# Kernel tuning notes

Hardware: AMD Instinct MI355X
Metric: run time of the kernel (lower is better)

## Reference

```python
import jax, jax.numpy as jnp
import numpy as np

W = 5      # window size
H = 4      # num heads (num_channels)
EPS = 1e-6

def rmsnorm(x, w):
    return x * w * jax.lax.rsqrt(jnp.mean(x * x, axis=-1, keepdims=True) + EPS)

def dwconv3d(x, k):
    # x: [B,D0,D1,D2,C], k: [3,3,3,1,C] depthwise 3x3x3 conv, SAME padding
    return jax.lax.conv_general_dilated(
        x, k, (1, 1, 1), 'SAME',
        dimension_numbers=('NDHWC', 'DHWIO', 'NDHWC'),
        feature_group_count=x.shape[-1])

def _part(t):
    # [B,D0,D1,D2,C] -> [B*nw, W^3, C] non-overlapping 3D windows
    B, D0, D1, D2, C = t.shape
    t = t.reshape(B, D0 // W, W, D1 // W, W, D2 // W, W, C)
    t = t.transpose(0, 1, 3, 5, 2, 4, 6, 7)
    return t.reshape(-1, W ** 3, C)

def _unpart(t, B, D0, D1, D2):
    C = t.shape[-1]
    t = t.reshape(B, D0 // W, D1 // W, D2 // W, W, W, W, C)
    t = t.transpose(0, 1, 4, 2, 5, 3, 6, 7)
    return t.reshape(B, D0, D1, D2, C)

def _pool01(t):
    # mean-pool poolable_dims=(0,1) by factor W -> coarse grid
    B, D0, D1, D2, C = t.shape
    return t.reshape(B, D0 // W, W, D1 // W, W, D2, C).mean(axis=(2, 4))

def _mha(q, k, v):
    # q,k,v: [N, L, C] -> [N, L, C] multi-head attention
    N, L, C = q.shape
    dh = C // H
    q = q.reshape(N, L, H, dh)
    k = k.reshape(N, L, H, dh)
    v = v.reshape(N, L, H, dh)
    s = jnp.einsum('nqhd,nkhd->nhqk', q, k) * (1.0 / np.sqrt(dh))
    p = jax.nn.softmax(s, axis=-1)
    return jnp.einsum('nhqk,nkhd->nqhd', p, v).reshape(N, L, C)

def _hier_attn(x, qkv_w, qkv_b, proj_w, proj_b, dw_pre, dw_post, lr_down, lr_up):
    B, D0, D1, D2, C = x.shape
    # conv_position='both': pre depthwise-conv positional term
    xin = x + dwconv3d(x, dw_pre)
    qkv = xin @ qkv_w + qkv_b                     # [B,D0,D1,D2,3C]
    q, k, v = jnp.split(qkv, 3, axis=-1)
    # fine scale: windowed local attention in W^3 blocks
    fine = _unpart(_mha(_part(q), _part(k), _part(v)), B, D0, D1, D2)
    # coarse scale: pool dims (0,1) by W, global attention over coarse tokens
    qc, kc, vc = _pool01(q), _pool01(k), _pool01(v)
    Nc = qc.shape[1] * qc.shape[2] * qc.shape[3]
    oc = _mha(qc.reshape(B, Nc, C), kc.reshape(B, Nc, C), vc.reshape(B, Nc, C))
    oc = oc.reshape(B, D0 // W, D1 // W, D2, C)
    oc = jnp.repeat(jnp.repeat(oc, W, axis=1), W, axis=2)   # upsample to full grid
    # lowrank hierarchical merge of coarse branch into fine branch
    merged = fine + (oc @ lr_down) @ lr_up
    out = merged @ proj_w + proj_b
    out = out + xin                               # attn_residual
    out = out + dwconv3d(out, dw_post)            # post conv position
    return out

def setup_inputs() -> dict:
    key = jax.random.key(0)
    ks = jax.random.split(key, 8)
    B, D0, D1, D2, C = 4, 40, 40, 20, 256
    rank = C // 4
    s = 0.02
    return {
        'x': jax.random.normal(ks[0], (B, D0, D1, D2, C), jnp.float32),
        'norm1_w': jnp.ones((C,), jnp.float32),
        'attn_norm_w': jnp.ones((C,), jnp.float32),
        'qkv_w': jax.random.normal(ks[1], (C, 3 * C), jnp.float32) * s,
        'qkv_b': jnp.zeros((3 * C,), jnp.float32),
        'proj_w': jax.random.normal(ks[2], (C, C), jnp.float32) * s,
        'proj_b': jnp.zeros((C,), jnp.float32),
        'dw_pre': jax.random.normal(ks[3], (3, 3, 3, 1, C), jnp.float32) * s,
        'dw_post': jax.random.normal(ks[4], (3, 3, 3, 1, C), jnp.float32) * s,
        'lr_down': jax.random.normal(ks[5], (C, rank), jnp.float32) * s,
        'lr_up': jax.random.normal(ks[6], (rank, C), jnp.float32) * s,
    }

def reference(x, norm1_w, attn_norm_w, qkv_w, qkv_b, proj_w, proj_b,
              dw_pre, dw_post, lr_down, lr_up) -> jnp.ndarray:
    # x = x + attn_norm(hier_attn(norm1(x)))   (dropout inactive in eval)
    a = _hier_attn(rmsnorm(x, norm1_w), qkv_w, qkv_b, proj_w, proj_b,
                   dw_pre, dw_post, lr_down, lr_up)
    return x + rmsnorm(a, attn_norm_w)
```

## Files before the change

kernel.cpp:

```cpp
#include <hip/hip_runtime.h>

#define D0c 40
#define D1c 40
#define D2c 20
#define NVOX 128000

typedef __attribute__((ext_vector_type(4))) float f4;
typedef __attribute__((ext_vector_type(8))) __bf16 bf8;
typedef __attribute__((ext_vector_type(8))) unsigned short u8s;

static __device__ __forceinline__ unsigned short f2bf(float f) {
  union { float f; unsigned int u; } v; v.f = f;
  unsigned int r = v.u + 0x7fffu + ((v.u >> 16) & 1u);
  return (unsigned short)(r >> 16);
}
static __device__ __forceinline__ float bf2f(unsigned short h) {
  union { unsigned int u; float f; } v; v.u = ((unsigned int)h) << 16;
  return v.f;
}

#define MFMA16(a, b, c) __builtin_amdgcn_mfma_f32_16x16x32_bf16((a), (b), (c), 0, 0, 0)

static __device__ __forceinline__ void gload16(const void* g, void* l) {
  __builtin_amdgcn_global_load_lds((const __attribute__((address_space(1))) unsigned int*)g,
                                   (__attribute__((address_space(3))) unsigned int*)l, 16, 0, 0);
}

#define CONV_LOAD(NB, R)                                                      \
  do {                                                                        \
    _Pragma("unroll") for (int c = 0; c < 9; c++)                             \
        NB[c] = *(const ushort4*)(base[c] + (size_t)(R) * 256);               \
  } while (0)

#define CONV_CONSUME(NB)                                                      \
  do {                                                                        \
    f4 cf[9];                                                                 \
    _Pragma("unroll") for (int c = 0; c < 9; c++) {                           \
      cf[c].x = bf2f(NB[c].x); cf[c].y = bf2f(NB[c].y);                       \
      cf[c].z = bf2f(NB[c].z); cf[c].w = bf2f(NB[c].w);                       \
    }                                                                         \
    _Pragma("unroll") for (int c = 0; c < 9; c++) {                           \
      const f4 w0 = *(const f4*)&wl[(c * 3 + 0) * 256 + c0];                  \
      const f4 w1 = *(const f4*)&wl[(c * 3 + 1) * 256 + c0];                  \
      const f4 w2 = *(const f4*)&wl[(c * 3 + 2) * 256 + c0];                  \
      a0 += w2 * cf[c]; a1 += w1 * cf[c]; a2 += w0 * cf[c];                   \
    }                                                                         \
    a1 += cf[4];                                                              \
  } while (0)

#define CONV_SHIFT()                                                          \
  do { a0 = a1; a1 = a2; a2 = (f4){0.f, 0.f, 0.f, 0.f}; } while (0)

__global__ __launch_bounds__(256) void k_prepw(const float* __restrict__ qkv_w,
                                               const float* __restrict__ proj_w,
                                               unsigned short* __restrict__ wq,
                                               unsigned short* __restrict__ wp,
                                               unsigned short* __restrict__ zpad) {
  if (blockIdx.x == 1024) {
    u8s z = {0, 0, 0, 0, 0, 0, 0, 0};
    for (int i = threadIdx.x; i < 768; i += 256) *(u8s*)(zpad + i * 8) = z;
    return;
  }
  int id = blockIdx.x * 256 + threadIdx.x;
  if (id < 768 * 256) {
    int kk = id & 31, row = (id >> 5) & 127, kc = (id >> 12) & 7, nt = id >> 15;
    int s = kk >> 3, kj = kk & 7;
    int g = s ^ ((row >> 1) & 3);
    int k = kc * 32 + g * 8 + kj;
    int n = nt * 128 + row;
    wq[id] = f2bf(qkv_w[k * 768 + n]);
  } else {
    int j = id - 768 * 256;
    int kk = j & 31, row = (j >> 5) & 127, kc = (j >> 12) & 7, nt = j >> 15;
    int s = kk >> 3, kj = kk & 7;
    int g = s ^ ((row >> 1) & 3);
    int k = kc * 32 + g * 8 + kj;
    int n = nt * 128 + row;
    wp[j] = f2bf(proj_w[k * 256 + n]);
  }
}

__global__ __launch_bounds__(256) void k_rms1(const float* __restrict__ x,
                                              const float* __restrict__ w,
                                              unsigned short* __restrict__ xn) {
  int wv = threadIdx.x >> 6, ln = threadIdx.x & 63;
  int n = blockIdx.x * 4 + wv;
  f4 v = ((const f4*)(x + (size_t)n * 256))[ln];
  float ss = v.x * v.x + v.y * v.y + v.z * v.z + v.w * v.w;
#pragma unroll
  for (int m = 32; m >= 1; m >>= 1) ss += __shfl_xor(ss, m);
  float rs = rsqrtf(ss * (1.f / 256.f) + 1e-6f);
  f4 wv4 = ((const f4*)w)[ln];
  ushort4 o;
  o.x = f2bf(v.x * wv4.x * rs); o.y = f2bf(v.y * wv4.y * rs);
  o.z = f2bf(v.z * wv4.z * rs); o.w = f2bf(v.w * wv4.w * rs);
  ((ushort4*)(xn + (size_t)n * 256))[ln] = o;
}

__global__ __launch_bounds__(256) void k_convpre(const unsigned short* __restrict__ xn,
                                                 const float* __restrict__ dw,
                                                 const unsigned short* __restrict__ zpad,
                                                 unsigned short* __restrict__ xin) {
  __shared__ float wl[6912];
  for (int i = threadIdx.x; i < 6912; i += 256) wl[i] = dw[i];
  __syncthreads();
  int wv = threadIdx.x >> 6, ln = threadIdx.x & 63;
  int col = blockIdx.x * 4 + wv;
  int z1 = col % D1c; int t = col / D1c; int z0 = t % D0c; int b = t / D0c;
  int c0 = ln * 4;

  const unsigned short* base[9];
#pragma unroll
  for (int c = 0; c < 9; c++) {
    int dy = c / 3 - 1, dx = c % 3 - 1;
    int y0 = z0 + dy, y1 = z1 + dx;
    bool valid = ((unsigned)y0 < (unsigned)D0c) && ((unsigned)y1 < (unsigned)D1c);
    base[c] = valid ? (xn + ((size_t)((b * D0c + y0) * D1c + y1) * D2c) * 256 + c0)
                    : (zpad + c0);
  }
  f4 a0 = {0.f,0.f,0.f,0.f}, a1 = {0.f,0.f,0.f,0.f}, a2 = {0.f,0.f,0.f,0.f};
  ushort4 n0[9], n1[9];
  CONV_LOAD(n0, 0);
  CONV_LOAD(n1, 1);
  unsigned short* op = xin + ((size_t)col * D2c) * 256 + c0;

  CONV_CONSUME(n0);
  CONV_SHIFT();
  CONV_LOAD(n0, 2);
  CONV_CONSUME(n1);
  {
    ushort4 o;
    o.x = f2bf(a0.x); o.y = f2bf(a0.y); o.z = f2bf(a0.z); o.w = f2bf(a0.w);
    *(ushort4*)op = o; op += 256;
  }
  CONV_SHIFT();
  CONV_LOAD(n1, 3);

  for (int z = 2; z < 20; z += 2) {
    CONV_CONSUME(n0);
    {
      ushort4 o;
      o.x = f2bf(a0.x); o.y = f2bf(a0.y); o.z = f2bf(a0.z); o.w = f2bf(a0.w);
      *(ushort4*)op = o; op += 256;
    }
    CONV_SHIFT();
    int r2 = (z + 2 > 19) ? 19 : (z + 2);
    CONV_LOAD(n0, r2);

    CONV_CONSUME(n1);
    {
      ushort4 o;
      o.x = f2bf(a0.x); o.y = f2bf(a0.y); o.z = f2bf(a0.z); o.w = f2bf(a0.w);
      *(ushort4*)op = o; op += 256;
    }
    CONV_SHIFT();
    int r3 = (z + 3 > 19) ? 19 : (z + 3);
    CONV_LOAD(n1, r3);
  }
  {
    ushort4 o;
    o.x = f2bf(a0.x); o.y = f2bf(a0.y); o.z = f2bf(a0.z); o.w = f2bf(a0.w);
    *(ushort4*)op = o;
  }
}

__global__ __launch_bounds__(512) void k_gemm_qkv(const unsigned short* __restrict__ a_bf,
                                                  const unsigned short* __restrict__ wq2,
                                                  const float* __restrict__ bias,
                                                  unsigned short* __restrict__ out) {
  __shared__ unsigned short As[32768];
  __shared__ unsigned short Bs[8192];
  int m0 = blockIdx.x * 128;
  int tid = threadIdx.x;
  int w = tid >> 6, l = tid & 63;
  int wr = w >> 1, wc = w & 1;
  int lrow = l & 15, lg = l >> 4;

  {
    const char* Ab = (const char*)(a_bf + (size_t)m0 * 256);
    int row = tid >> 2, s = tid & 3;
    int g = s ^ ((row >> 1) & 3);
    const char* src0 = Ab + row * 512 + g * 16;
    char* dst0 = ((char*)As) + w * 1024 + l * 16;
#pragma unroll
    for (int kc = 0; kc < 8; kc++)
      gload16(src0 + kc * 64, dst0 + kc * 8192);
  }
  gload16(((const char*)wq2) + tid * 16, ((char*)Bs) + tid * 16);

  f4 acc[2][4];
  int crow = tid >> 4, cs8 = (tid & 15) * 8;
  for (int nt = 0; nt < 6; nt++) {
    float bvv[4];
#pragma unroll
    for (int j = 0; j < 4; j++) bvv[j] = bias[nt * 128 + wc * 64 + j * 16 + lrow];
#pragma unroll
    for (int i = 0; i < 2; i++)
#pragma unroll
      for (int j = 0; j < 4; j++) acc[i][j] = {0.f, 0.f, 0.f, 0.f};

    for (int kc = 0; kc < 8; kc++) {
      int t = nt * 8 + kc;
      asm volatile("s_barrier" ::: "memory");
      if (t + 1 < 48) {
        gload16(((const char*)wq2) + (size_t)(t + 1) * 8192 + tid * 16,
                ((char*)Bs) + (size_t)((t + 1) & 1) * 8192 + tid * 16);
        asm volatile("s_waitcnt vmcnt(1)" ::: "memory");
      } else {
        asm volatile("s_waitcnt vmcnt(0)" ::: "memory");
      }
      int buf = t & 1;
      bf8 af[2], bf_[4];
#pragma unroll
      for (int i = 0; i < 2; i++) {
        int row = wr * 32 + i * 16 + lrow;
        af[i] = *(const bf8*)&As[kc * 4096 + row * 32 + ((lg ^ ((row >> 1) & 3)) * 8)];
      }
#pragma unroll
      for (int j = 0; j < 4; j++) {
        int rowb = wc * 64 + j * 16 + lrow;
        bf_[j] = *(const bf8*)&Bs[buf * 4096 + rowb * 32 + ((lg ^ ((rowb >> 1) & 3)) * 8)];
      }
#pragma unroll
      for (int i = 0; i < 2; i++)
#pragma unroll
        for (int j = 0; j < 4; j++) acc[i][j] = MFMA16(af[i], bf_[j], acc[i][j]);
    }

    asm volatile("s_barrier" ::: "memory");
    unsigned short* Cs = &Bs[4096];
#pragma unroll
    for (int h = 0; h < 4; h++) {
      if (wr == h) {
#pragma unroll
        for (int i = 0; i < 2; i++)
#pragma unroll
          for (int j = 0; j < 4; j++)
#pragma unroll
            for (int r = 0; r < 4; r++)
              Cs[(i * 16 + lg * 4 + r) * 128 + wc * 64 + j * 16 + lrow] =
                  f2bf(acc[i][j][r] + bvv[j]);
      }
      asm volatile("s_waitcnt lgkmcnt(0)\n\ts_barrier" ::: "memory");
      {
        u8s v0 = *(const u8s*)&Cs[crow * 128 + cs8];
        unsigned short* orow = out + (size_t)(m0 + h * 32 + crow) * 768 + nt * 128 + cs8;
        *(u8s*)orow = v0;
      }
      asm volatile("s_waitcnt lgkmcnt(0)\n\ts_barrier" ::: "memory");
    }
  }
}

__global__ __launch_bounds__(256) void k_fineattn(const unsigned short* __restrict__ qkv,
                                                  unsigned short* __restrict__ fine) {
  __shared__ unsigned short sm[27136];
  unsigned short* Qs = sm;
  unsigned short* Ks = sm + 9216;
  unsigned short* Vt = sm + 18432;
  unsigned short* Ps = sm;
  int h = blockIdx.x & 3, wid = blockIdx.x >> 2;
  int w2 = wid & 3, w1 = (wid >> 2) & 7, w0 = (wid >> 5) & 7, b = wid >> 8;
  int tid = threadIdx.x;
  int tok = tid >> 1, half = tid & 1;
  if (tok < 125) {
    int i0 = tok / 25, rr = tok % 25, i1 = rr / 5, i2 = rr % 5;
    int n = ((b * D0c + w0 * 5 + i0) * D1c + w1 * 5 + i1) * D2c + w2 * 5 + i2;
    const u8s* qp = (const u8s*)(qkv + (size_t)n * 768 + h * 64 + half * 32);
    const u8s* kp = (const u8s*)(qkv + (size_t)n * 768 + 256 + h * 64 + half * 32);
    const unsigned short* vp = qkv + (size_t)n * 768 + 512 + h * 64 + half * 32;
#pragma unroll
    for (int e = 0; e < 4; e++) {
      *(u8s*)&Qs[tok * 72 + half * 32 + e * 8] = qp[e];
      *(u8s*)&Ks[tok * 72 + half * 32 + e * 8] = kp[e];
    }
#pragma unroll
    for (int d = 0; d < 32; d++) Vt[(half * 32 + d) * 136 + tok] = vp[d];
  } else {
    u8s z = {0, 0, 0, 0, 0, 0, 0, 0};
#pragma unroll
    for (int e = 0; e < 4; e++) {
      *(u8s*)&Qs[tok * 72 + half * 32 + e * 8] = z;
      *(u8s*)&Ks[tok * 72 + half * 32 + e * 8] = z;
    }
#pragma unroll
    for (int d = 0; d < 32; d++) Vt[(half * 32 + d) * 136 + tok] = 0;
  }
  __syncthreads();
  int wv = tid >> 6, ln = tid & 63, lrow = ln & 15, lg = ln >> 4;
  f4 s[2][8];
#pragma unroll
  for (int mi = 0; mi < 2; mi++)
#pragma unroll
    for (int ni = 0; ni < 8; ni++) s[mi][ni] = {0.f, 0.f, 0.f, 0.f};
  bf8 aq[2][2];
#pragma unroll
  for (int ks = 0; ks < 2; ks++)
#pragma unroll
    for (int mi = 0; mi < 2; mi++)
      aq[mi][ks] = *(const bf8*)&Qs[(wv * 32 + mi * 16 + lrow) * 72 + ks * 32 + lg * 8];
#pragma unroll
  for (int ni = 0; ni < 8; ni++) {
#pragma unroll
    for (int ks = 0; ks < 2; ks++) {
      bf8 bk = *(const bf8*)&Ks[(ni * 16 + lrow) * 72 + ks * 32 + lg * 8];
      s[0][ni] = MFMA16(aq[0][ks], bk, s[0][ni]);
      s[1][ni] = MFMA16(aq[1][ks], bk, s[1][ni]);
    }
  }
#pragma unroll
  for (int mi = 0; mi < 2; mi++) {
#pragma unroll
    for (int j = 0; j < 4; j++) {
      float mx = -3e38f;
#pragma unroll
      for (int ni = 0; ni < 8; ni++) {
        int col = ni * 16 + lrow;
        float v = (col < 125) ? s[mi][ni][j] * 0.125f : -3e38f;
        s[mi][ni][j] = v;
        mx = fmaxf(mx, v);
      }
#pragma unroll
      for (int m = 8; m >= 1; m >>= 1) mx = fmaxf(mx, __shfl_xor(mx, m));
      float sum = 0.f;
#pragma unroll
      for (int ni = 0; ni < 8; ni++) {
        float p = __expf(s[mi][ni][j] - mx);
        s[mi][ni][j] = p;
        sum += p;
      }
#pragma unroll
      for (int m = 8; m >= 1; m >>= 1) sum += __shfl_xor(sum, m);
      float inv = 1.f / sum;
#pragma unroll
      for (int ni = 0; ni < 8; ni++) s[mi][ni][j] *= inv;
    }
  }
  __syncthreads();
#pragma unroll
  for (int mi = 0; mi < 2; mi++)
#pragma unroll
    for (int ni = 0; ni < 8; ni++)
#pragma unroll
      for (int j = 0; j < 4; j++)
        Ps[(wv * 32 + mi * 16 + lg * 4 + j) * 136 + ni * 16 + lrow] = f2bf(s[mi][ni][j]);
  __syncthreads();
  f4 o[2][4];
#pragma unroll
  for (int mi = 0; mi < 2; mi++)
#pragma unroll
    for (int ni = 0; ni < 4; ni++) o[mi][ni] = {0.f, 0.f, 0.f, 0.f};
#pragma unroll
  for (int ks = 0; ks < 4; ks++) {
    bf8 ap0 = *(const bf8*)&Ps[(wv * 32 + 0 + lrow) * 136 + ks * 32 + lg * 8];
    bf8 ap1 = *(const bf8*)&Ps[(wv * 32 + 16 + lrow) * 136 + ks * 32 + lg * 8];
#pragma unroll
    for (int ni = 0; ni < 4; ni++) {
      bf8 bv = *(const bf8*)&Vt[(ni * 16 + lrow) * 136 + ks * 32 + lg * 8];
      o[0][ni] = MFMA16(ap0, bv, o[0][ni]);
      o[1][ni] = MFMA16(ap1, bv, o[1][ni]);
    }
  }
#pragma unroll
  for (int mi = 0; mi < 2; mi++) {
    int rt0 = wv * 32 + mi * 16 + lg * 4;
#pragma unroll
    for (int r = 0; r < 4; r++) {
      int tk = rt0 + r;
      if (tk >= 125) continue;
      int i0 = tk / 25, rr = tk % 25, i1 = rr / 5, i2 = rr % 5;
      int n = ((b * D0c + w0 * 5 + i0) * D1c + w1 * 5 + i1) * D2c + w2 * 5 + i2;
#pragma unroll
      for (int ni = 0; ni < 4; ni++)
        fine[(size_t)n * 256 + h * 64 + ni * 16 + lrow] = f2bf(o[mi][ni][r]);
    }
  }
}

__global__ __launch_bounds__(128) void k_pool(const unsigned short* __restrict__ qkv,
                                              unsigned short* __restrict__ qc,
                                              unsigned short* __restrict__ kc,
                                              unsigned short* __restrict__ vct) {
  int ct = blockIdx.x;
  int tid = threadIdx.x;
  if (tid >= 96) return;
  int z2 = ct % 20; int t = ct / 20; int c1 = t & 7; int c0 = (t >> 3) & 7; int b = t >> 6;
  int off = tid * 8;
  f4 s0 = {0.f, 0.f, 0.f, 0.f}, s1 = {0.f, 0.f, 0.f, 0.f};
  for (int i0 = 0; i0 < 5; i0++)
    for (int i1 = 0; i1 < 5; i1++) {
      int n = ((b * D0c + c0 * 5 + i0) * D1c + c1 * 5 + i1) * D2c + z2;
      u8s v = *(const u8s*)(qkv + (size_t)n * 768 + off);
      s0.x += bf2f(v[0]); s0.y += bf2f(v[1]); s0.z += bf2f(v[2]); s0.w += bf2f(v[3]);
      s1.x += bf2f(v[4]); s1.y += bf2f(v[5]); s1.z += bf2f(v[6]); s1.w += bf2f(v[7]);
    }
  const float sc = 1.f / 25.f;
  s0.x *= sc; s0.y *= sc; s0.z *= sc; s0.w *= sc;
  s1.x *= sc; s1.y *= sc; s1.z *= sc; s1.w *= sc;
  if (off < 512) {
    unsigned short* dst = (off < 256) ? (qc + (size_t)ct * 256 + off)
                                      : (kc + (size_t)ct * 256 + (off - 256));
    u8s o;
    o[0] = f2bf(s0.x); o[1] = f2bf(s0.y); o[2] = f2bf(s0.z); o[3] = f2bf(s0.w);
    o[4] = f2bf(s1.x); o[5] = f2bf(s1.y); o[6] = f2bf(s1.z); o[7] = f2bf(s1.w);
    *(u8s*)dst = o;
  } else {
    int vch = off - 512;
    int h = vch >> 6, d0 = vch & 63;
    int tk = ct - b * 1280;
    unsigned short* vb = vct + (((size_t)b * 4 + h) * 64 + d0) * 1288 + tk;
    vb[0 * 1288] = f2bf(s0.x); vb[1 * 1288] = f2bf(s0.y);
    vb[2 * 1288] = f2bf(s0.z); vb[3 * 1288] = f2bf(s0.w);
    vb[4 * 1288] = f2bf(s1.x); vb[5 * 1288] = f2bf(s1.y);
    vb[6 * 1288] = f2bf(s1.z); vb[7 * 1288] = f2bf(s1.w);
  }
}

__global__ __launch_bounds__(256) void k_coarse(const unsigned short* __restrict__ qc,
                                                const unsigned short* __restrict__ kc,
                                                const unsigned short* __restrict__ vct,
                                                float* __restrict__ oc) {
  __shared__ unsigned short Qs[9216];
  __shared__ unsigned short KP[9216];
  __shared__ unsigned short Vts[4608];
  int qt = blockIdx.x;
  int b = blockIdx.y >> 2, h = blockIdx.y & 3;
  int tid = threadIdx.x, wv = tid >> 6, ln = tid & 63, lrow = ln & 15, lg = ln >> 4;
  {
    int tk = tid >> 1, half = tid & 1;
    const u8s* qp = (const u8s*)(qc + (size_t)(b * 1280 + qt * 128 + tk) * 256 + h * 64 + half * 32);
#pragma unroll
    for (int e = 0; e < 4; e++) *(u8s*)&Qs[tk * 72 + half * 32 + e * 8] = qp[e];
  }
  float mrun[2][4], srun[2][4];
  f4 o[2][4];
#pragma unroll
  for (int mi = 0; mi < 2; mi++)
#pragma unroll
    for (int j = 0; j < 4; j++) { mrun[mi][j] = -3e38f; srun[mi][j] = 0.f; }
#pragma unroll
  for (int mi = 0; mi < 2; mi++)
#pragma unroll
    for (int ni = 0; ni < 4; ni++) o[mi][ni] = {0.f, 0.f, 0.f, 0.f};

  int ktok = tid >> 2, kq = (tid & 3) * 16;
  int vd = tid >> 2, vtc = (tid & 3) * 16;

  for (int kt = 0; kt < 20; kt++) {
    {
      const u8s* kp = (const u8s*)(kc + (size_t)(b * 1280 + kt * 64 + ktok) * 256 + h * 64 + kq);
      *(u8s*)&KP[ktok * 72 + kq] = kp[0];
      *(u8s*)&KP[ktok * 72 + kq + 8] = kp[1];
      const u8s* vp = (const u8s*)(vct + (((size_t)b * 4 + h) * 64 + vd) * 1288 + kt * 64 + vtc);
      *(u8s*)&Vts[vd * 72 + vtc] = vp[0];
      *(u8s*)&Vts[vd * 72 + vtc + 8] = vp[1];
    }
    __syncthreads();
    f4 s[2][4];
#pragma unroll
    for (int mi = 0; mi < 2; mi++)
#pragma unroll
      for (int ni = 0; ni < 4; ni++) s[mi][ni] = {0.f, 0.f, 0.f, 0.f};
    bf8 aq[2][2];
#pragma unroll
    for (int ks = 0; ks < 2; ks++)
#pragma unroll
      for (int mi = 0; mi < 2; mi++)
        aq[mi][ks] = *(const bf8*)&Qs[(wv * 32 + mi * 16 + lrow) * 72 + ks * 32 + lg * 8];
#pragma unroll
    for (int ni = 0; ni < 4; ni++) {
#pragma unroll
      for (int ks = 0; ks < 2; ks++) {
        bf8 bk = *(const bf8*)&KP[(ni * 16 + lrow) * 72 + ks * 32 + lg * 8];
        s[0][ni] = MFMA16(aq[0][ks], bk, s[0][ni]);
        s[1][ni] = MFMA16(aq[1][ks], bk, s[1][ni]);
      }
    }
#pragma unroll
    for (int mi = 0; mi < 2; mi++) {
#pragma unroll
      for (int j = 0; j < 4; j++) {
        float mx = -3e38f;
#pragma unroll
        for (int ni = 0; ni < 4; ni++) {
          float v = s[mi][ni][j] * 0.125f;
          s[mi][ni][j] = v;
          mx = fmaxf(mx, v);
        }
#pragma unroll
        for (int m = 8; m >= 1; m >>= 1) mx = fmaxf(mx, __shfl_xor(mx, m));
        float nm = fmaxf(mrun[mi][j], mx);
        float alpha = __expf(mrun[mi][j] - nm);
        mrun[mi][j] = nm;
        float sum = 0.f;
#pragma unroll
        for (int ni = 0; ni < 4; ni++) {
          float p = __expf(s[mi][ni][j] - nm);
          s[mi][ni][j] = p;
          sum += p;
        }
#pragma unroll
        for (int m = 8; m >= 1; m >>= 1) sum += __shfl_xor(sum, m);
        srun[mi][j] = srun[mi][j] * alpha + sum;
#pragma unroll
        for (int ni = 0; ni < 4; ni++) o[mi][ni][j] *= alpha;
      }
    }
    __syncthreads();
#pragma unroll
    for (int mi = 0; mi < 2; mi++)
#pragma unroll
      for (int ni = 0; ni < 4; ni++)
#pragma unroll
        for (int j = 0; j < 4; j++)
          KP[(wv * 32 + mi * 16 + lg * 4 + j) * 72 + ni * 16 + lrow] = f2bf(s[mi][ni][j]);
    __syncthreads();
#pragma unroll
    for (int ks = 0; ks < 2; ks++) {
      bf8 ap0 = *(const bf8*)&KP[(wv * 32 + 0 + lrow) * 72 + ks * 32 + lg * 8];
      bf8 ap1 = *(const bf8*)&KP[(wv * 32 + 16 + lrow) * 72 + ks * 32 + lg * 8];
#pragma unroll
      for (int ni = 0; ni < 4; ni++) {
        bf8 bv = *(const bf8*)&Vts[(ni * 16 + lrow) * 72 + ks * 32 + lg * 8];
        o[0][ni] = MFMA16(ap0, bv, o[0][ni]);
        o[1][ni] = MFMA16(ap1, bv, o[1][ni]);
      }
    }
    __syncthreads();
  }
#pragma unroll
  for (int mi = 0; mi < 2; mi++)
#pragma unroll
    for (int j = 0; j < 4; j++) {
      float inv = 1.f / srun[mi][j];
      int row = qt * 128 + wv * 32 + mi * 16 + lg * 4 + j;
      float* orow = oc + ((size_t)(b * 1280 + row)) * 256 + h * 64;
#pragma unroll
      for (int ni = 0; ni < 4; ni++) orow[ni * 16 + lrow] = o[mi][ni][j] * inv;
    }
}

__global__ __launch_bounds__(256) void k_lowrank(const float* __restrict__ oc,
                                                 const float* __restrict__ lrd,
                                                 const float* __restrict__ lru,
                                                 float* __restrict__ oclr) {
  __shared__ float tmp[16 * 64];
  int t0 = blockIdx.x * 16;
  int tid = threadIdx.x;
  int i = tid >> 4, r4 = (tid & 15) * 4;
  f4 a = {0.f, 0.f, 0.f, 0.f};
  const float* orow = oc + (size_t)(t0 + i) * 256;
  for (int k = 0; k < 256; k++) {
    float ov = orow[k];
    const f4 w = *(const f4*)&lrd[k * 64 + r4];
    a.x += ov * w.x; a.y += ov * w.y; a.z += ov * w.z; a.w += ov * w.w;
  }
  *(f4*)&tmp[i * 64 + r4] = a;
  __syncthreads();
  int c16 = (tid & 15) * 16;
  f4 acc0 = {0.f,0.f,0.f,0.f}, acc1 = {0.f,0.f,0.f,0.f}, acc2 = {0.f,0.f,0.f,0.f}, acc3 = {0.f,0.f,0.f,0.f};
  for (int r = 0; r < 64; r++) {
    float tv = tmp[i * 64 + r];
    const f4* wr = (const f4*)&lru[r * 256 + c16];
    f4 w0 = wr[0], w1 = wr[1], w2 = wr[2], w3 = wr[3];
    acc0.x += tv * w0.x; acc0.y += tv * w0.y; acc0.z += tv * w0.z; acc0.w += tv * w0.w;
    acc1.x += tv * w1.x; acc1.y += tv * w1.y; acc1.z += tv * w1.z; acc1.w += tv * w1.w;
    acc2.x += tv * w2.x; acc2.y += tv * w2.y; acc2.z += tv * w2.z; acc2.w += tv * w2.w;
    acc3.x += tv * w3.x; acc3.y += tv * w3.y; acc3.z += tv * w3.z; acc3.w += tv * w3.w;
  }
  float* outr = oclr + (size_t)(t0 + i) * 256 + c16;
  *(f4*)&outr[0] = acc0; *(f4*)&outr[4] = acc1; *(f4*)&outr[8] = acc2; *(f4*)&outr[12] = acc3;
}

__global__ __launch_bounds__(256) void k_gemm_proj(const unsigned short* __restrict__ fine,
                                                   const float* __restrict__ oclr,
                                                   const unsigned short* __restrict__ wp2,
                                                   const float* __restrict__ bias,
                                                   const unsigned short* __restrict__ xin,
                                                   unsigned short* __restrict__ out1) {
  __shared__ unsigned short As[16384];
  __shared__ unsigned short Bs[8192];
  int m0 = blockIdx.x * 64;
  int tid = threadIdx.x;
  int w = tid >> 6, l = tid & 63;
  int wr = w >> 1, wc = w & 1;
  int lrow = l & 15, lg = l >> 4;

  {
    const char* gB = (const char*)wp2;
    char* lB = (char*)Bs;
    gload16(gB + tid * 16, lB + w * 1024 + l * 16);
    gload16(gB + 4096 + tid * 16, lB + 4096 + w * 1024 + l * 16);
  }
  {
    int row = tid >> 2, s = tid & 3;
    int g = s ^ ((row >> 1) & 3);
    int nrow = m0 + row;
    int z2 = nrow % D2c; int tt = nrow / D2c; int z1 = tt % D1c; tt /= D1c;
    int z0 = tt % D0c; int bb = tt / D0c;
    int ct = ((bb * 8 + z0 / 5) * 8 + z1 / 5) * 20 + z2;
    const unsigned short* fp = fine + (size_t)nrow * 256 + g * 8;
    const float* cp = oclr + (size_t)ct * 256 + g * 8;
#pragma unroll
    for (int kc = 0; kc < 8; kc++) {
      u8s fv = *(const u8s*)(fp + kc * 32);
      f4 cv0 = *(const f4*)(cp + kc * 32);
      f4 cv1 = *(const f4*)(cp + kc * 32 + 4);
      u8s t0;
      t0[0] = f2bf(bf2f(fv[0]) + cv0.x); t0[1] = f2bf(bf2f(fv[1]) + cv0.y);
      t0[2] = f2bf(bf2f(fv[2]) + cv0.z); t0[3] = f2bf(bf2f(fv[3]) + cv0.w);
      t0[4] = f2bf(bf2f(fv[4]) + cv1.x); t0[5] = f2bf(bf2f(fv[5]) + cv1.y);
      t0[6] = f2bf(bf2f(fv[6]) + cv1.z); t0[7] = f2bf(bf2f(fv[7]) + cv1.w);
      *(u8s*)&As[kc * 2048 + row * 32 + s * 8] = t0;
    }
  }
  asm volatile("s_waitcnt lgkmcnt(0)\n\ts_barrier" ::: "memory");

  int buf = 0;
  f4 acc[2][4];
  for (int nt = 0; nt < 2; nt++) {
    float bvv[4];
#pragma unroll
    for (int j = 0; j < 4; j++) bvv[j] = bias[nt * 128 + wc * 64 + j * 16 + lrow];
#pragma unroll
    for (int i = 0; i < 2; i++)
#pragma unroll
      for (int j = 0; j < 4; j++) acc[i][j] = {0.f, 0.f, 0.f, 0.f};

    for (int kc = 0; kc < 8; kc++) {
      int t = nt * 8 + kc;
      if (t + 1 < 16) {
        const char* gB = (const char*)wp2 + (size_t)(t + 1) * 8192;
        char* lB = ((char*)Bs) + (buf ^ 1) * 8192;
        gload16(gB + tid * 16, lB + w * 1024 + l * 16);
        gload16(gB + 4096 + tid * 16, lB + 4096 + w * 1024 + l * 16);
        asm volatile("s_waitcnt vmcnt(2)\n\ts_barrier" ::: "memory");
      } else {
        asm volatile("s_waitcnt vmcnt(0)\n\ts_barrier" ::: "memory");
      }
      bf8 af[2], bf_[4];
#pragma unroll
      for (int i = 0; i < 2; i++) {
        int row = wr * 32 + i * 16 + lrow;
        af[i] = *(const bf8*)&As[kc * 2048 + row * 32 + ((lg ^ ((row >> 1) & 3)) * 8)];
      }
#pragma unroll
      for (int j = 0; j < 4; j++) {
        int rowb = wc * 64 + j * 16 + lrow;
        bf_[j] = *(const bf8*)&Bs[buf * 4096 + rowb * 32 + ((lg ^ ((rowb >> 1) & 3)) * 8)];
      }
#pragma unroll
      for (int i = 0; i < 2; i++)
#pragma unroll
        for (int j = 0; j < 4; j++) acc[i][j] = MFMA16(af[i], bf_[j], acc[i][j]);
      asm volatile("s_barrier" ::: "memory");
      buf ^= 1;
    }

    unsigned short* Cs = &Bs[(buf ^ 1) * 4096];
    int crow = tid >> 3, cseg = tid & 7;
#pragma unroll
    for (int h = 0; h < 2; h++) {
      if (wr == h) {
#pragma unroll
        for (int i = 0; i < 2; i++)
#pragma unroll
          for (int j = 0; j < 4; j++)
#pragma unroll
            for (int r = 0; r < 4; r++)
              Cs[(i * 16 + lg * 4 + r) * 128 + wc * 64 + j * 16 + lrow] =
                  f2bf(acc[i][j][r] + bvv[j]);
      }
      asm volatile("s_waitcnt lgkmcnt(0)\n\ts_barrier" ::: "memory");
      {
        u8s v0 = *(const u8s*)&Cs[crow * 128 + cseg * 16];
        u8s v1 = *(const u8s*)&Cs[crow * 128 + cseg * 16 + 8];
        const unsigned short* xrow = xin + (size_t)(m0 + h * 32 + crow) * 256 + nt * 128 + cseg * 16;
        u8s x0 = *(const u8s*)xrow;
        u8s x1 = *(const u8s*)(xrow + 8);
        u8s o0, o1;
#pragma unroll
        for (int e = 0; e < 8; e++) {
          o0[e] = f2bf(bf2f(v0[e]) + bf2f(x0[e]));
          o1[e] = f2bf(bf2f(v1[e]) + bf2f(x1[e]));
        }
        unsigned short* orow = out1 + (size_t)(m0 + h * 32 + crow) * 256 + nt * 128 + cseg * 16;
        *(u8s*)orow = o0;
        *(u8s*)(orow + 8) = o1;
      }
      asm volatile("s_waitcnt lgkmcnt(0)\n\ts_barrier" ::: "memory");
    }
  }
}

__global__ __launch_bounds__(256) void k_convpost(const unsigned short* __restrict__ o1,
                                                  const float* __restrict__ dw,
                                                  const unsigned short* __restrict__ zpad,
                                                  const float* __restrict__ x,
                                                  const float* __restrict__ anw,
                                                  float* __restrict__ outp) {
  __shared__ float wl[6912];
  for (int i = threadIdx.x; i < 6912; i += 256) wl[i] = dw[i];
  __syncthreads();
  int wv = threadIdx.x >> 6, ln = threadIdx.x & 63;
  int col = blockIdx.x * 4 + wv;
  int z1 = col % D1c; int t = col / D1c; int z0 = t % D0c; int b = t / D0c;
  int c0 = ln * 4;

  const unsigned short* base[9];
#pragma unroll
  for (int c = 0; c < 9; c++) {
    int dy = c / 3 - 1, dx = c % 3 - 1;
    int y0 = z0 + dy, y1 = z1 + dx;
    bool valid = ((unsigned)y0 < (unsigned)D0c) && ((unsigned)y1 < (unsigned)D1c);
    base[c] = valid ? (o1 + ((size_t)((b * D0c + y0) * D1c + y1) * D2c) * 256 + c0)
                    : (zpad + c0);
  }
  f4 a0 = {0.f,0.f,0.f,0.f}, a1 = {0.f,0.f,0.f,0.f}, a2 = {0.f,0.f,0.f,0.f};
  ushort4 n0[9], n1[9];
  CONV_LOAD(n0, 0);
  CONV_LOAD(n1, 1);
  const f4 wv4 = *(const f4*)(anw + c0);
  const float* xp = x + ((size_t)col * D2c) * 256 + c0;
  float* op = outp + ((size_t)col * D2c) * 256 + c0;

#define POST_STORE()                                                          \
  do {                                                                        \
    float ss = a0.x * a0.x + a0.y * a0.y + a0.z * a0.z + a0.w * a0.w;         \
    _Pragma("unroll") for (int m = 32; m >= 1; m >>= 1)                       \
        ss += __shfl_xor(ss, m);                                              \
    float rs = rsqrtf(ss * (1.f / 256.f) + 1e-6f);                            \
    f4 xv = *(const f4*)xp;                                                   \
    f4 res;                                                                   \
    res.x = xv.x + a0.x * wv4.x * rs;                                         \
    res.y = xv.y + a0.y * wv4.y * rs;                                         \
    res.z = xv.z + a0.z * wv4.z * rs;                                         \
    res.w = xv.w + a0.w * wv4.w * rs;                                         \
    *(f4*)op = res;                                                           \
    xp += 256; op += 256;                                                     \
  } while (0)

  CONV_CONSUME(n0);
  CONV_SHIFT();
  CONV_LOAD(n0, 2);
  CONV_CONSUME(n1);
  POST_STORE();
  CONV_SHIFT();
  CONV_LOAD(n1, 3);

  for (int z = 2; z < 20; z += 2) {
    CONV_CONSUME(n0);
    POST_STORE();
    CONV_SHIFT();
    int r2 = (z + 2 > 19) ? 19 : (z + 2);
    CONV_LOAD(n0, r2);

    CONV_CONSUME(n1);
    POST_STORE();
    CONV_SHIFT();
    int r3 = (z + 3 > 19) ? 19 : (z + 3);
    CONV_LOAD(n1, r3);
  }
  POST_STORE();
#undef POST_STORE
}

extern "C" void kernel_launch(void* const* d_in, const int* in_sizes, int n_in,
                              void* d_out, int out_size, void* d_ws, size_t ws_size,
                              hipStream_t stream) {
  const float* x          = (const float*)d_in[0];
  const float* norm1_w    = (const float*)d_in[1];
  const float* attn_norm_w= (const float*)d_in[2];
  const float* qkv_w      = (const float*)d_in[3];
  const float* qkv_b      = (const float*)d_in[4];
  const float* proj_w     = (const float*)d_in[5];
  const float* proj_b     = (const float*)d_in[6];
  const float* dw_pre     = (const float*)d_in[7];
  const float* dw_post    = (const float*)d_in[8];
  const float* lr_down    = (const float*)d_in[9];
  const float* lr_up      = (const float*)d_in[10];
  float* outp = (float*)d_out;

  unsigned char* w = (unsigned char*)d_ws;
  size_t off = 0;
  unsigned short* xn   = (unsigned short*)(w + off); off += 65536000ULL;
  unsigned short* xin  = (unsigned short*)(w + off); off += 65536000ULL;
  unsigned short* qkv  = (unsigned short*)(w + off); off += 196608000ULL;
  unsigned short* out1 = (unsigned short*)(w + off); off += 65536000ULL;
  unsigned short* qc   = (unsigned short*)(w + off); off += 2621440ULL;
  unsigned short* kc   = (unsigned short*)(w + off); off += 2621440ULL;
  unsigned short* vct  = (unsigned short*)(w + off); off += 2637824ULL;
  float* oc            = (float*)(w + off);          off += 5242880ULL;
  float* oclr          = (float*)(w + off);          off += 5242880ULL;
  unsigned short* wq   = (unsigned short*)(w + off); off += 393216ULL;
  unsigned short* wp   = (unsigned short*)(w + off); off += 131072ULL;
  unsigned short* zpad = (unsigned short*)(w + off); off += 12288ULL;
  unsigned short* fine = xn;

  k_prepw<<<1025, 256, 0, stream>>>(qkv_w, proj_w, wq, wp, zpad);
  k_rms1<<<32000, 256, 0, stream>>>(x, norm1_w, xn);
  k_convpre<<<1600, 256, 0, stream>>>(xn, dw_pre, zpad, xin);
  k_gemm_qkv<<<1000, 512, 0, stream>>>(xin, wq, qkv_b, qkv);
  k_fineattn<<<4096, 256, 0, stream>>>(qkv, fine);
  k_pool<<<5120, 128, 0, stream>>>(qkv, qc, kc, vct);
  k_coarse<<<dim3(10, 16), 256, 0, stream>>>(qc, kc, vct, oc);
  k_lowrank<<<320, 256, 0, stream>>>(oc, lr_down, lr_up, oclr);
  k_gemm_proj<<<2000, 256, 0, stream>>>(fine, oclr, wp, proj_b, xin, out1);
  k_convpost<<<1600, 256, 0, stream>>>(out1, dw_post, zpad, x, attn_norm_w, outp);
}
```

Baseline: 597.5 us.

## Split depthwise convs along z into two blocks; hoist A fragments into registers in QKV GEMM

Both depthwise 3D conv kernels now launch a second grid dimension that splits the 20-deep z axis into two halves of 10. Each block loads its own halo rows, with zero padding at the volume boundary, which doubles the number of blocks and improves occupancy and latency hiding. The cost is re-reading two halo rows per column. Separately, the QKV GEMM loads all A-tile fragments into registers once before the N-tile loop instead of re-reading them from LDS each iteration, and adds a launch-bounds occupancy hint; this raises register pressure.

```diff
diff --git a/kernel.cpp b/kernel.cpp
--- a/kernel.cpp
+++ b/kernel.cpp
@@ -26,10 +26,14 @@
                                    (__attribute__((address_space(3))) unsigned int*)l, 16, 0, 0);
 }
 
-#define CONV_LOAD(NB, R)                                                      \
+#define CONV_LOADZ(NB, R)                                                     \
   do {                                                                        \
-    _Pragma("unroll") for (int c = 0; c < 9; c++)                             \
-        NB[c] = *(const ushort4*)(base[c] + (size_t)(R) * 256);               \
+    bool zok_ = ((unsigned)(R) < 20u);                                        \
+    _Pragma("unroll") for (int c = 0; c < 9; c++) {                           \
+      const unsigned short* p_ =                                              \
+          zok_ ? (base[c] + (size_t)(R) * 256) : (zpad + c0);                 \
+      NB[c] = *(const ushort4*)p_;                                            \
+    }                                                                         \
   } while (0)
 
 #define CONV_CONSUME(NB)                                                      \
@@ -106,6 +110,7 @@
   __syncthreads();
   int wv = threadIdx.x >> 6, ln = threadIdx.x & 63;
   int col = blockIdx.x * 4 + wv;
+  int zs = blockIdx.y * 10;
   int z1 = col % D1c; int t = col / D1c; int z0 = t % D0c; int b = t / D0c;
   int c0 = ln * 4;
 
@@ -120,23 +125,18 @@
   }
   f4 a0 = {0.f,0.f,0.f,0.f}, a1 = {0.f,0.f,0.f,0.f}, a2 = {0.f,0.f,0.f,0.f};
   ushort4 n0[9], n1[9];
-  CONV_LOAD(n0, 0);
-  CONV_LOAD(n1, 1);
-  unsigned short* op = xin + ((size_t)col * D2c) * 256 + c0;
+  CONV_LOADZ(n0, zs - 1);
+  CONV_LOADZ(n1, zs);
+  unsigned short* op = xin + ((size_t)col * D2c + zs) * 256 + c0;
 
   CONV_CONSUME(n0);
   CONV_SHIFT();
-  CONV_LOAD(n0, 2);
+  CONV_LOADZ(n0, zs + 1);
   CONV_CONSUME(n1);
-  {
-    ushort4 o;
-    o.x = f2bf(a0.x); o.y = f2bf(a0.y); o.z = f2bf(a0.z); o.w = f2bf(a0.w);
-    *(ushort4*)op = o; op += 256;
-  }
   CONV_SHIFT();
-  CONV_LOAD(n1, 3);
-
-  for (int z = 2; z < 20; z += 2) {
+  CONV_LOADZ(n1, zs + 2);
+#pragma unroll
+  for (int s = 2; s < 12; s += 2) {
     CONV_CONSUME(n0);
     {
       ushort4 o;
@@ -144,8 +144,7 @@
       *(ushort4*)op = o; op += 256;
     }
     CONV_SHIFT();
-    int r2 = (z + 2 > 19) ? 19 : (z + 2);
-    CONV_LOAD(n0, r2);
+    if (s < 10) CONV_LOADZ(n0, zs + s + 1);
 
     CONV_CONSUME(n1);
     {
@@ -154,20 +153,14 @@
       *(ushort4*)op = o; op += 256;
     }
     CONV_SHIFT();
-    int r3 = (z + 3 > 19) ? 19 : (z + 3);
-    CONV_LOAD(n1, r3);
-  }
-  {
-    ushort4 o;
-    o.x = f2bf(a0.x); o.y = f2bf(a0.y); o.z = f2bf(a0.z); o.w = f2bf(a0.w);
-    *(ushort4*)op = o;
-  }
-}
-
-__global__ __launch_bounds__(512) void k_gemm_qkv(const unsigned short* __restrict__ a_bf,
-                                                  const unsigned short* __restrict__ wq2,
-                                                  const float* __restrict__ bias,
-                                                  unsigned short* __restrict__ out) {
+    if (s < 10) CONV_LOADZ(n1, zs + s + 2);
+  }
+}
+
+__global__ __launch_bounds__(512, 4) void k_gemm_qkv(const unsigned short* __restrict__ a_bf,
+                                                     const unsigned short* __restrict__ wq2,
+                                                     const float* __restrict__ bias,
+                                                     unsigned short* __restrict__ out) {
   __shared__ unsigned short As[32768];
   __shared__ unsigned short Bs[8192];
   int m0 = blockIdx.x * 128;
@@ -187,6 +180,16 @@
       gload16(src0 + kc * 64, dst0 + kc * 8192);
   }
   gload16(((const char*)wq2) + tid * 16, ((char*)Bs) + tid * 16);
+
+  asm volatile("s_waitcnt vmcnt(1)\n\ts_barrier" ::: "memory");
+  bf8 afr[2][8];
+#pragma unroll
+  for (int i = 0; i < 2; i++)
+#pragma unroll
+    for (int kc = 0; kc < 8; kc++) {
+      int row = wr * 32 + i * 16 + lrow;
+      afr[i][kc] = *(const bf8*)&As[kc * 4096 + row * 32 + ((lg ^ ((row >> 1) & 3)) * 8)];
+    }
 
   f4 acc[2][4];
   int crow = tid >> 4, cs8 = (tid & 15) * 8;
@@ -210,12 +213,7 @@
         asm volatile("s_waitcnt vmcnt(0)" ::: "memory");
       }
       int buf = t & 1;
-      bf8 af[2], bf_[4];
-#pragma unroll
-      for (int i = 0; i < 2; i++) {
-        int row = wr * 32 + i * 16 + lrow;
-        af[i] = *(const bf8*)&As[kc * 4096 + row * 32 + ((lg ^ ((row >> 1) & 3)) * 8)];
-      }
+      bf8 bf_[4];
 #pragma unroll
       for (int j = 0; j < 4; j++) {
         int rowb = wc * 64 + j * 16 + lrow;
@@ -224,7 +222,7 @@
 #pragma unroll
       for (int i = 0; i < 2; i++)
 #pragma unroll
-        for (int j = 0; j < 4; j++) acc[i][j] = MFMA16(af[i], bf_[j], acc[i][j]);
+        for (int j = 0; j < 4; j++) acc[i][j] = MFMA16(afr[i][kc], bf_[j], acc[i][j]);
     }
 
     asm volatile("s_barrier" ::: "memory");
@@ -704,6 +702,7 @@
   __syncthreads();
   int wv = threadIdx.x >> 6, ln = threadIdx.x & 63;
   int col = blockIdx.x * 4 + wv;
+  int zs = blockIdx.y * 10;
   int z1 = col % D1c; int t = col / D1c; int z0 = t % D0c; int b = t / D0c;
   int c0 = ln * 4;
 
@@ -718,11 +717,11 @@
   }
   f4 a0 = {0.f,0.f,0.f,0.f}, a1 = {0.f,0.f,0.f,0.f}, a2 = {0.f,0.f,0.f,0.f};
   ushort4 n0[9], n1[9];
-  CONV_LOAD(n0, 0);
-  CONV_LOAD(n1, 1);
+  CONV_LOADZ(n0, zs - 1);
+  CONV_LOADZ(n1, zs);
   const f4 wv4 = *(const f4*)(anw + c0);
-  const float* xp = x + ((size_t)col * D2c) * 256 + c0;
-  float* op = outp + ((size_t)col * D2c) * 256 + c0;
+  const float* xp = x + ((size_t)col * D2c + zs) * 256 + c0;
+  float* op = outp + ((size_t)col * D2c + zs) * 256 + c0;
 
 #define POST_STORE()                                                          \
   do {                                                                        \
@@ -742,26 +741,22 @@
 
   CONV_CONSUME(n0);
   CONV_SHIFT();
-  CONV_LOAD(n0, 2);
+  CONV_LOADZ(n0, zs + 1);
   CONV_CONSUME(n1);
-  POST_STORE();
   CONV_SHIFT();
-  CONV_LOAD(n1, 3);
-
-  for (int z = 2; z < 20; z += 2) {
+  CONV_LOADZ(n1, zs + 2);
+#pragma unroll
+  for (int s = 2; s < 12; s += 2) {
     CONV_CONSUME(n0);
     POST_STORE();
     CONV_SHIFT();
-    int r2 = (z + 2 > 19) ? 19 : (z + 2);
-    CONV_LOAD(n0, r2);
+    if (s < 10) CONV_LOADZ(n0, zs + s + 1);
 
     CONV_CONSUME(n1);
     POST_STORE();
     CONV_SHIFT();
-    int r3 = (z + 3 > 19) ? 19 : (z + 3);
-    CONV_LOAD(n1, r3);
-  }
-  POST_STORE();
+    if (s < 10) CONV_LOADZ(n1, zs + s + 2);
+  }
 #undef POST_STORE
 }
 
@@ -799,12 +794,12 @@
 
   k_prepw<<<1025, 256, 0, stream>>>(qkv_w, proj_w, wq, wp, zpad);
   k_rms1<<<32000, 256, 0, stream>>>(x, norm1_w, xn);
-  k_convpre<<<1600, 256, 0, stream>>>(xn, dw_pre, zpad, xin);
+  k_convpre<<<dim3(1600, 2), 256, 0, stream>>>(xn, dw_pre, zpad, xin);
   k_gemm_qkv<<<1000, 512, 0, stream>>>(xin, wq, qkv_b, qkv);
   k_fineattn<<<4096, 256, 0, stream>>>(qkv, fine);
   k_pool<<<5120, 128, 0, stream>>>(qkv, qc, kc, vct);
   k_coarse<<<dim3(10, 16), 256, 0, stream>>>(qc, kc, vct, oc);
   k_lowrank<<<320, 256, 0, stream>>>(oc, lr_down, lr_up, oclr);
   k_gemm_proj<<<2000, 256, 0, stream>>>(fine, oclr, wp, proj_b, xin, out1);
-  k_convpost<<<1600, 256, 0, stream>>>(out1, dw_post, zpad, x, attn_norm_w, outp);
-}
+  k_convpost<<<dim3(1600, 2), 256, 0, stream>>>(out1, dw_post, zpad, x, attn_norm_w, outp);
+}
```

Result: slower. 710.7 us (+19.0%).
